# Kernel optimization log

Hardware: AMD Instinct MI355X
Metric: run time of the kernel (lower is better)

## Reference

```python
import jax, jax.numpy as jnp
import numpy as np
from jax import lax

B, N, C, W, D = 128, 16384, 8, 10, 3   # batch, input_size, n_channels, out_window, poly_degree
L = N - W + 1                          # in-filter tap length
EPS = 1e-5


def setup_inputs() -> dict:
    key = jax.random.key(0)
    ks = jax.random.split(key, 8)
    x = jax.random.normal(ks[0], (B, N, C, 2), dtype=jnp.float32)
    # torch Linear-style scale ~ 1/sqrt(fan_in)
    w_in_real = jax.random.normal(ks[1], (C, L), dtype=jnp.float32) * (L ** -0.5)
    w_in_imag = jax.random.normal(ks[2], (C, L), dtype=jnp.float32) * (L ** -0.5)
    fan_coeff = 2 * (C - 1) * D
    w_coeff = jax.random.normal(ks[3], (C, 2, fan_coeff), dtype=jnp.float32) * (fan_coeff ** -0.5)
    w_out_real = jax.random.normal(ks[4], (C, W), dtype=jnp.float32) * (W ** -0.5)
    w_out_imag = jax.random.normal(ks[5], (C, W), dtype=jnp.float32) * (W ** -0.5)
    bn_gamma = jnp.ones((C,), dtype=jnp.float32)
    bn_beta = jnp.zeros((C,), dtype=jnp.float32)
    return {"x": x, "w_in_real": w_in_real, "w_in_imag": w_in_imag,
            "w_coeff": w_coeff, "w_out_real": w_out_real,
            "w_out_imag": w_out_imag, "bn_gamma": bn_gamma, "bn_beta": bn_beta}


# complement index map: row c lists all channels != c
_IDX = np.array([[j for j in range(C) if j != c] for c in range(C)])  # (C, C-1)


def _grouped_fir(sig, w):
    # sig: (B, N, C); per-channel length-L correlation -> (B, W, C)
    out = lax.conv_general_dilated(
        jnp.transpose(sig, (0, 2, 1)),      # (B, C, N)
        w[:, None, :],                      # (C, 1, L)
        window_strides=(1,), padding='VALID', feature_group_count=C)
    return jnp.transpose(out, (0, 2, 1))    # (B, W, C)


def reference(x, w_in_real, w_in_imag, w_coeff, w_out_real, w_out_imag, bn_gamma, bn_beta):
    fr = _grouped_fir(x[..., 0], w_in_real)   # (B, W, C)
    fi = _grouped_fir(x[..., 1], w_in_imag)   # (B, W, C)

    # polynomial expansion: pow_d = fr^d + fi^d, d = 1..D
    powd = jnp.stack([fr ** d + fi ** d for d in range(1, D + 1)], axis=-1)  # (B, W, C, D)
    poly_r = powd * fr[..., None]
    poly_i = powd * fi[..., None]

    # cross-channel coeff layers: input layout = [real(all j != c), imag(all j != c)]
    rg = poly_r[:, :, _IDX, :]                      # (B, W, C, C-1, D)
    ig = poly_i[:, :, _IDX, :]
    Wc = w_coeff.reshape(C, 2, 2, C - 1, D)         # (c, out, real/imag half, j, d)
    nonlin = (jnp.einsum('bwcjd,cpjd->bwcp', rg, Wc[:, :, 0]) +
              jnp.einsum('bwcjd,cpjd->bwcp', ig, Wc[:, :, 1]))  # (B, W, C, 2)

    out_r = jnp.einsum('bwc,cw->bc', nonlin[..., 0], w_out_real)
    out_i = jnp.einsum('bwc,cw->bc', nonlin[..., 1], w_out_imag)
    out = jnp.stack([out_r, out_i], axis=-1)        # (B, C, 2)

    # BatchNorm1d over (batch, last) per channel, training-mode batch stats
    mean = out.mean(axis=(0, 2), keepdims=True)
    var = out.var(axis=(0, 2), keepdims=True)
    return (out - mean) / jnp.sqrt(var + EPS) * bn_gamma[None, :, None] + bn_beta[None, :, None]
```

## Files before the change

### kernel.cpp

```cpp
#include <hip/hip_runtime.h>

#define BB 128
#define NN 16384
#define CC 8
#define WW 10
#define LL 16375
#define NT 512
#define NTILES (NN / NT)
#define BT 4
#define BTILES (BB / BT)
#define WSL (NT + 9)
#define BPB 16
#define ABLK (BB / BPB)

typedef float f4_t __attribute__((ext_vector_type(4)));

__global__ __launch_bounds__(256) void k_fir(const float* __restrict__ x,
                                             const float* __restrict__ wr,
                                             const float* __restrict__ wi,
                                             float* __restrict__ fpart) {
  __shared__ float smem[WSL * 16 + 16];
  f4_t* sw = (f4_t*)smem;

  int nt = blockIdx.x & (NTILES - 1);
  int bt = blockIdx.x >> 5;
  int tid = threadIdx.x;
  int ntile = nt * NT;
  int l0 = ntile - 9;

  {
    int c2s = tid >> 6;
    int ca = 2 * c2s, cb = 2 * c2s + 1;
    for (int j = tid & 63; j < WSL; j += 64) {
      int l = l0 + j;
      f4_t v = (f4_t)0.f;
      if (l >= 0 && l < LL) {
        v[0] = wr[(size_t)ca * LL + l];
        v[1] = wi[(size_t)ca * LL + l];
        v[2] = wr[(size_t)cb * LL + l];
        v[3] = wi[(size_t)cb * LL + l];
      }
      sw[j * 4 + c2s] = v;
    }
  }
  __syncthreads();

  int c2   = tid & 3;
  int bsub = (tid >> 2) & 3;
  int nh   = tid >> 4;
  int b    = bt * BT + bsub;
  int n0   = ntile + nh * 32;

  const f4_t* __restrict__ xp = ((const f4_t*)x) + ((size_t)b * NN + n0) * 4 + c2;
  const f4_t* swp = sw + (nh * 32 + 9) * 4 + c2;

  f4_t acc[WW];
#pragma unroll
  for (int w = 0; w < WW; ++w) acc[w] = (f4_t)0.f;

  f4_t wv[16];
#pragma unroll
  for (int k = 0; k < 9; ++k) wv[7 + k] = swp[4 * (k - 9)];

#pragma unroll
  for (int g = 0; g < 2; ++g) {
#pragma unroll
    for (int j = 0; j < 7; ++j) wv[j] = swp[4 * (16 * g + j)];
#pragma unroll
    for (int u = 0; u < 16; ++u) {
      f4_t xv = xp[(size_t)(16 * g + u) * 4];
#pragma unroll
      for (int w = 0; w < WW; ++w) {
        f4_t wt = wv[(u - w + 16) & 15];
        acc[w][0] += xv[0] * wt[0];
        acc[w][1] += xv[1] * wt[1];
        acc[w][2] += xv[2] * wt[2];
        acc[w][3] += xv[3] * wt[3];
      }
      if (u <= 8) wv[u + 7] = swp[4 * (16 * g + u + 7)];
    }
  }

#pragma unroll
  for (int w = 0; w < WW; ++w)
#pragma unroll
    for (int e = 0; e < 4; ++e) {
      acc[w][e] += __shfl_xor(acc[w][e], 16);
      acc[w][e] += __shfl_xor(acc[w][e], 32);
    }

  __syncthreads();
  int wave = tid >> 6, lane = tid & 63;
  if (lane < 16) {
#pragma unroll
    for (int w = 0; w < WW; ++w)
      *(f4_t*)&smem[(wave * 16 + lane) * 40 + w * 4] = acc[w];
  }
  __syncthreads();
  for (int t = tid; t < BT * 160; t += 256) {
    int bs = t / 160;
    int r  = t - bs * 160;
    int w  = r >> 4;
    int cc = (r >> 1) & 7;
    int ri = r & 1;
    int ln = (cc >> 1) + 4 * bs;
    int e  = (cc & 1) * 2 + ri;
    float s = 0.f;
#pragma unroll
    for (int wv_ = 0; wv_ < 4; ++wv_) s += smem[(wv_ * 16 + ln) * 40 + w * 4 + e];
    fpart[((size_t)(bt * BT + bs) * NTILES + nt) * 160 + r] = s;
  }
}

__global__ __launch_bounds__(256) void k_nonlin(const float* __restrict__ fpart,
                                                const float* __restrict__ wc,
                                                const float* __restrict__ wor,
                                                const float* __restrict__ woi,
                                                float* __restrict__ oraw,
                                                float* __restrict__ part) {
  __shared__ float sred[BPB][164];
  __shared__ float swc[704];
  __shared__ float swout[160];

  int tid = threadIdx.x;
  int blk = blockIdx.x;
  int b0 = blk * BPB;

  for (int i = tid; i < 672; i += 256) swc[i] = wc[i];
  if (tid < 80) swout[tid] = wor[tid];
  else if (tid < 160) swout[tid] = woi[tid - 80];

  {
    const float4* fp4 = (const float4*)fpart;
    for (int o4 = tid; o4 < BPB * 40; o4 += 256) {
      int bl = o4 / 40;
      int r4 = o4 - bl * 40;
      float4 s = {0.f, 0.f, 0.f, 0.f};
      size_t base = ((size_t)(b0 + bl) * NTILES) * 40 + r4;
#pragma unroll
      for (int seg = 0; seg < NTILES; ++seg) {
        float4 v = fp4[base + (size_t)seg * 40];
        s.x += v.x; s.y += v.y; s.z += v.z; s.w += v.w;
      }
      int r = r4 * 4;
      sred[bl][r] = s.x; sred[bl][r + 1] = s.y; sred[bl][r + 2] = s.z; sred[bl][r + 3] = s.w;
    }
  }
  __syncthreads();

  int b = tid >> 4;
  int c = (tid >> 1) & 7;
  int p = tid & 1;

  float wreg[8][2][3];
#pragma unroll
  for (int j = 0; j < 8; ++j) {
    int jj = j - (j > c ? 1 : 0);
    if (j == c) jj = 0;
#pragma unroll
    for (int ri = 0; ri < 2; ++ri)
#pragma unroll
      for (int d = 0; d < 3; ++d) {
        float v = swc[(c * 2 + p) * 42 + ri * 21 + jj * 3 + d];
        wreg[j][ri][d] = (j == c) ? 0.f : v;
      }
  }

  float o = 0.f;
  const float* wop = swout + p * 80 + c * 10;
#pragma unroll
  for (int w = 0; w < WW; ++w) {
    float4 f0 = *(const float4*)&sred[b][w * 16];
    float4 f1 = *(const float4*)&sred[b][w * 16 + 4];
    float4 f2 = *(const float4*)&sred[b][w * 16 + 8];
    float4 f3 = *(const float4*)&sred[b][w * 16 + 12];
    float fv[16] = {f0.x, f0.y, f0.z, f0.w, f1.x, f1.y, f1.z, f1.w,
                    f2.x, f2.y, f2.z, f2.w, f3.x, f3.y, f3.z, f3.w};
    float nl0 = 0.f, nl1 = 0.f, nl2 = 0.f;
#pragma unroll
    for (int j = 0; j < 8; ++j) {
      float r  = fv[2 * j];
      float im = fv[2 * j + 1];
      float r2 = r * r, i2 = im * im;
      float pw0 = r + im;
      float pw1 = r2 + i2;
      float pw2 = r2 * r + i2 * im;
      nl0 += (pw0 * r) * wreg[j][0][0] + (pw0 * im) * wreg[j][1][0];
      nl1 += (pw1 * r) * wreg[j][0][1] + (pw1 * im) * wreg[j][1][1];
      nl2 += (pw2 * r) * wreg[j][0][2] + (pw2 * im) * wreg[j][1][2];
    }
    o += (nl0 + nl1 + nl2) * wop[w];
  }

  oraw[((size_t)(b0 + b) * CC + c) * 2 + p] = o;

  __shared__ float sval[256], ssq[256];
  sval[tid] = o;
  ssq[tid]  = o * o;
  __syncthreads();
  if (tid < 8) {
    float S = 0.f, Q = 0.f;
#pragma unroll
    for (int k = 0; k < 32; ++k) {
      int t = (k >> 1) * 16 + tid * 2 + (k & 1);
      S += sval[t];
      Q += ssq[t];
    }
    part[(blk * 8 + tid) * 2 + 0] = S;
    part[(blk * 8 + tid) * 2 + 1] = Q;
  }
}

__global__ __launch_bounds__(256) void k_bn(const float* __restrict__ oraw,
                                            const float* __restrict__ part,
                                            const float* __restrict__ gamma,
                                            const float* __restrict__ beta,
                                            float* __restrict__ out) {
  __shared__ float mv[8], iv[8], bv[8];
  int tid = threadIdx.x;
  if (tid < 8) {
    float S = 0.f, Q = 0.f;
#pragma unroll
    for (int blk = 0; blk < ABLK; ++blk) {
      S += part[(blk * 8 + tid) * 2 + 0];
      Q += part[(blk * 8 + tid) * 2 + 1];
    }
    float mean = S * (1.0f / 256.0f);
    float var  = Q * (1.0f / 256.0f) - mean * mean;
    mv[tid] = mean;
    iv[tid] = gamma[tid] * rsqrtf(var + 1e-5f);
    bv[tid] = beta[tid];
  }
  __syncthreads();
  for (int i = tid; i < BB * CC * 2; i += 256) {
    int c = (i >> 1) & 7;
    out[i] = (oraw[i] - mv[c]) * iv[c] + bv[c];
  }
}

extern "C" void kernel_launch(void* const* d_in, const int* in_sizes, int n_in,
                              void* d_out, int out_size, void* d_ws, size_t ws_size,
                              hipStream_t stream) {
  const float* x   = (const float*)d_in[0];
  const float* wr  = (const float*)d_in[1];
  const float* wi  = (const float*)d_in[2];
  const float* wc  = (const float*)d_in[3];
  const float* wor = (const float*)d_in[4];
  const float* woi = (const float*)d_in[5];
  const float* gm  = (const float*)d_in[6];
  const float* bt  = (const float*)d_in[7];
  float* out = (float*)d_out;

  float* ws    = (float*)d_ws;
  float* fpart = ws;
  float* oraw  = fpart + (size_t)BB * NTILES * 160;
  float* part  = oraw + BB * CC * 2;

  k_fir<<<dim3(BTILES * NTILES), dim3(256), 0, stream>>>(x, wr, wi, fpart);
  k_nonlin<<<dim3(ABLK), dim3(256), 0, stream>>>(fpart, wc, wor, woi, oraw, part);
  k_bn<<<dim3(1), dim3(256), 0, stream>>>(oraw, part, gm, bt, out);
}
```

Before: 45.52 us.

## Fuse batchnorm into nonlin kernel via last-block atomic counter, widen grid

Removes the separate batchnorm kernel launch by having the last finishing nonlin block (detected with an atomic counter reset in the FIR kernel) compute the statistics and write the normalized output. The nonlin grid is also widened from 8 to 64 blocks with 2 batches each, so the fpart reduction is spread across more CUs. The cost is atomics and threadfences, plus a serial tail in the final block. Only 32 threads per block do the nonlinear math now.

```diff
diff --git a/kernel.cpp b/kernel.cpp
--- a/kernel.cpp
+++ b/kernel.cpp
@@ -10,7 +10,7 @@
 #define BT 4
 #define BTILES (BB / BT)
 #define WSL (NT + 9)
-#define BPB 16
+#define BPB 2
 #define ABLK (BB / BPB)
 
 typedef float f4_t __attribute__((ext_vector_type(4)));
@@ -18,7 +18,10 @@
 __global__ __launch_bounds__(256) void k_fir(const float* __restrict__ x,
                                              const float* __restrict__ wr,
                                              const float* __restrict__ wi,
-                                             float* __restrict__ fpart) {
+                                             float* __restrict__ fpart,
+                                             unsigned int* __restrict__ cnt) {
+  if (blockIdx.x == 0 && threadIdx.x == 0) *cnt = 0u;
+
   __shared__ float smem[WSL * 16 + 16];
   f4_t* sw = (f4_t*)smem;
 
@@ -116,10 +119,14 @@
                                                 const float* __restrict__ wc,
                                                 const float* __restrict__ wor,
                                                 const float* __restrict__ woi,
+                                                const float* __restrict__ gamma,
+                                                const float* __restrict__ beta,
                                                 float* __restrict__ oraw,
-                                                float* __restrict__ part) {
+                                                float* __restrict__ part,
+                                                unsigned int* __restrict__ cnt,
+                                                float* __restrict__ out) {
   __shared__ float sred[BPB][164];
-  __shared__ float swc[704];
+  __shared__ float swc[672];
   __shared__ float swout[160];
 
   int tid = threadIdx.x;
@@ -130,111 +137,105 @@
   if (tid < 80) swout[tid] = wor[tid];
   else if (tid < 160) swout[tid] = woi[tid - 80];
 
-  {
+  if (tid < BPB * 40) {
+    int bl = tid / 40;
+    int r4 = tid - bl * 40;
     const float4* fp4 = (const float4*)fpart;
-    for (int o4 = tid; o4 < BPB * 40; o4 += 256) {
-      int bl = o4 / 40;
-      int r4 = o4 - bl * 40;
-      float4 s = {0.f, 0.f, 0.f, 0.f};
-      size_t base = ((size_t)(b0 + bl) * NTILES) * 40 + r4;
-#pragma unroll
-      for (int seg = 0; seg < NTILES; ++seg) {
-        float4 v = fp4[base + (size_t)seg * 40];
-        s.x += v.x; s.y += v.y; s.z += v.z; s.w += v.w;
-      }
-      int r = r4 * 4;
-      sred[bl][r] = s.x; sred[bl][r + 1] = s.y; sred[bl][r + 2] = s.z; sred[bl][r + 3] = s.w;
-    }
-  }
-  __syncthreads();
-
-  int b = tid >> 4;
-  int c = (tid >> 1) & 7;
-  int p = tid & 1;
-
-  float wreg[8][2][3];
-#pragma unroll
-  for (int j = 0; j < 8; ++j) {
-    int jj = j - (j > c ? 1 : 0);
-    if (j == c) jj = 0;
-#pragma unroll
-    for (int ri = 0; ri < 2; ++ri)
-#pragma unroll
-      for (int d = 0; d < 3; ++d) {
-        float v = swc[(c * 2 + p) * 42 + ri * 21 + jj * 3 + d];
-        wreg[j][ri][d] = (j == c) ? 0.f : v;
-      }
-  }
-
-  float o = 0.f;
-  const float* wop = swout + p * 80 + c * 10;
-#pragma unroll
-  for (int w = 0; w < WW; ++w) {
-    float4 f0 = *(const float4*)&sred[b][w * 16];
-    float4 f1 = *(const float4*)&sred[b][w * 16 + 4];
-    float4 f2 = *(const float4*)&sred[b][w * 16 + 8];
-    float4 f3 = *(const float4*)&sred[b][w * 16 + 12];
-    float fv[16] = {f0.x, f0.y, f0.z, f0.w, f1.x, f1.y, f1.z, f1.w,
-                    f2.x, f2.y, f2.z, f2.w, f3.x, f3.y, f3.z, f3.w};
-    float nl0 = 0.f, nl1 = 0.f, nl2 = 0.f;
+    float4 s = {0.f, 0.f, 0.f, 0.f};
+    size_t base = ((size_t)(b0 + bl) * NTILES) * 40 + r4;
+#pragma unroll
+    for (int seg = 0; seg < NTILES; ++seg) {
+      float4 v = fp4[base + (size_t)seg * 40];
+      s.x += v.x; s.y += v.y; s.z += v.z; s.w += v.w;
+    }
+    int r = r4 * 4;
+    sred[bl][r] = s.x; sred[bl][r + 1] = s.y; sred[bl][r + 2] = s.z; sred[bl][r + 3] = s.w;
+  }
+  __syncthreads();
+
+  if (tid < 32) {
+    int bl = tid >> 4;
+    int c  = (tid >> 1) & 7;
+    int p  = tid & 1;
+
+    float wreg[8][2][3];
 #pragma unroll
     for (int j = 0; j < 8; ++j) {
-      float r  = fv[2 * j];
-      float im = fv[2 * j + 1];
-      float r2 = r * r, i2 = im * im;
-      float pw0 = r + im;
-      float pw1 = r2 + i2;
-      float pw2 = r2 * r + i2 * im;
-      nl0 += (pw0 * r) * wreg[j][0][0] + (pw0 * im) * wreg[j][1][0];
-      nl1 += (pw1 * r) * wreg[j][0][1] + (pw1 * im) * wreg[j][1][1];
-      nl2 += (pw2 * r) * wreg[j][0][2] + (pw2 * im) * wreg[j][1][2];
-    }
-    o += (nl0 + nl1 + nl2) * wop[w];
-  }
-
-  oraw[((size_t)(b0 + b) * CC + c) * 2 + p] = o;
-
-  __shared__ float sval[256], ssq[256];
-  sval[tid] = o;
-  ssq[tid]  = o * o;
-  __syncthreads();
-  if (tid < 8) {
-    float S = 0.f, Q = 0.f;
-#pragma unroll
-    for (int k = 0; k < 32; ++k) {
-      int t = (k >> 1) * 16 + tid * 2 + (k & 1);
-      S += sval[t];
-      Q += ssq[t];
-    }
-    part[(blk * 8 + tid) * 2 + 0] = S;
-    part[(blk * 8 + tid) * 2 + 1] = Q;
-  }
-}
-
-__global__ __launch_bounds__(256) void k_bn(const float* __restrict__ oraw,
-                                            const float* __restrict__ part,
-                                            const float* __restrict__ gamma,
-                                            const float* __restrict__ beta,
-                                            float* __restrict__ out) {
-  __shared__ float mv[8], iv[8], bv[8];
-  int tid = threadIdx.x;
-  if (tid < 8) {
-    float S = 0.f, Q = 0.f;
-#pragma unroll
-    for (int blk = 0; blk < ABLK; ++blk) {
-      S += part[(blk * 8 + tid) * 2 + 0];
-      Q += part[(blk * 8 + tid) * 2 + 1];
-    }
-    float mean = S * (1.0f / 256.0f);
-    float var  = Q * (1.0f / 256.0f) - mean * mean;
-    mv[tid] = mean;
-    iv[tid] = gamma[tid] * rsqrtf(var + 1e-5f);
-    bv[tid] = beta[tid];
-  }
-  __syncthreads();
-  for (int i = tid; i < BB * CC * 2; i += 256) {
-    int c = (i >> 1) & 7;
-    out[i] = (oraw[i] - mv[c]) * iv[c] + bv[c];
+      int jj = j - (j > c ? 1 : 0);
+      if (j == c) jj = 0;
+#pragma unroll
+      for (int ri = 0; ri < 2; ++ri)
+#pragma unroll
+        for (int d = 0; d < 3; ++d) {
+          float v = swc[(c * 2 + p) * 42 + ri * 21 + jj * 3 + d];
+          wreg[j][ri][d] = (j == c) ? 0.f : v;
+        }
+    }
+
+    float o = 0.f;
+    const float* wop = swout + p * 80 + c * 10;
+#pragma unroll
+    for (int w = 0; w < WW; ++w) {
+      float4 f0 = *(const float4*)&sred[bl][w * 16];
+      float4 f1 = *(const float4*)&sred[bl][w * 16 + 4];
+      float4 f2 = *(const float4*)&sred[bl][w * 16 + 8];
+      float4 f3 = *(const float4*)&sred[bl][w * 16 + 12];
+      float fv[16] = {f0.x, f0.y, f0.z, f0.w, f1.x, f1.y, f1.z, f1.w,
+                      f2.x, f2.y, f2.z, f2.w, f3.x, f3.y, f3.z, f3.w};
+      float nl0 = 0.f, nl1 = 0.f, nl2 = 0.f;
+#pragma unroll
+      for (int j = 0; j < 8; ++j) {
+        float r  = fv[2 * j];
+        float im = fv[2 * j + 1];
+        float r2 = r * r, i2 = im * im;
+        float pw0 = r + im;
+        float pw1 = r2 + i2;
+        float pw2 = r2 * r + i2 * im;
+        nl0 += (pw0 * r) * wreg[j][0][0] + (pw0 * im) * wreg[j][1][0];
+        nl1 += (pw1 * r) * wreg[j][0][1] + (pw1 * im) * wreg[j][1][1];
+        nl2 += (pw2 * r) * wreg[j][0][2] + (pw2 * im) * wreg[j][1][2];
+      }
+      o += (nl0 + nl1 + nl2) * wop[w];
+    }
+
+    oraw[((size_t)(b0 + bl) * CC + c) * 2 + p] = o;
+
+    float s = o, q = o * o;
+    s += __shfl_xor(s, 1);  q += __shfl_xor(q, 1);
+    s += __shfl_xor(s, 16); q += __shfl_xor(q, 16);
+    if ((tid & 17) == 0) {
+      part[blk * 16 + c * 2 + 0] = s;
+      part[blk * 16 + c * 2 + 1] = q;
+    }
+  }
+
+  __threadfence();
+  __syncthreads();
+  __shared__ int lastFlag;
+  if (tid == 0) lastFlag = (atomicAdd(cnt, 1u) == (unsigned)(ABLK - 1)) ? 1 : 0;
+  __syncthreads();
+  if (lastFlag) {
+    __threadfence();
+    __shared__ float mv[8], ivv[8], bvv[8];
+    if (tid < 16) {
+      int cc = tid >> 1, qq = tid & 1;
+      float s = 0.f;
+#pragma unroll
+      for (int k = 0; k < ABLK; ++k) s += part[k * 16 + cc * 2 + qq];
+      float other = __shfl_xor(s, 1);
+      if (qq == 0) {
+        float mean = s * (1.0f / 256.0f);
+        float var  = other * (1.0f / 256.0f) - mean * mean;
+        mv[cc]  = mean;
+        ivv[cc] = gamma[cc] * rsqrtf(var + 1e-5f);
+        bvv[cc] = beta[cc];
+      }
+    }
+    __syncthreads();
+    for (int i = tid; i < BB * CC * 2; i += 256) {
+      int cc = (i >> 1) & 7;
+      out[i] = (oraw[i] - mv[cc]) * ivv[cc] + bvv[cc];
+    }
   }
 }
 
@@ -255,8 +256,9 @@
   float* fpart = ws;
   float* oraw  = fpart + (size_t)BB * NTILES * 160;
   float* part  = oraw + BB * CC * 2;
-
-  k_fir<<<dim3(BTILES * NTILES), dim3(256), 0, stream>>>(x, wr, wi, fpart);
-  k_nonlin<<<dim3(ABLK), dim3(256), 0, stream>>>(fpart, wc, wor, woi, oraw, part);
-  k_bn<<<dim3(1), dim3(256), 0, stream>>>(oraw, part, gm, bt, out);
+  unsigned int* cnt = (unsigned int*)(part + ABLK * 16);
+
+  k_fir<<<dim3(BTILES * NTILES), dim3(256), 0, stream>>>(x, wr, wi, fpart, cnt);
+  k_nonlin<<<dim3(ABLK), dim3(256), 0, stream>>>(fpart, wc, wor, woi, gm, bt,
+                                                 oraw, part, cnt, out);
 }
```

Measured after the change: 45.24 us. No clear change (-0.6%).
